# Optimization experiments

Hardware: AMD Instinct MI355X
Metric: run time of the kernel (lower is better)

Reference implementation:

```python
import jax, jax.numpy as jnp
import numpy as np

NUM_TOTAL = 150000
NUM_USER = 50000
NUM_ITEM = NUM_TOTAL - NUM_USER
D = 128
SOC_L = 2
CO_L = 2
NEG = 10
R = 0.7
E_SOC = 1600000
E_CO = 3200000
B = 512
MAX_UI = 64
MAX_IU = 50
W = 32
HOP = 3


def _sage_lgcn(x, src, dst, w, n, layers):
    # SAGEConv with edge-softmax weights over destination (LGCN 'mean' option).
    m = jax.lax.stop_gradient(jax.ops.segment_max(w, dst, num_segments=n))
    e = jnp.exp(w - m[dst])
    s = jax.ops.segment_sum(e, dst, num_segments=n)
    alpha = e / (s[dst] + 1e-16)
    for _ in range(layers):
        x = jax.ops.segment_sum(alpha[:, None] * x[src], dst, num_segments=n)
    return x  # LGCN.forward returns the last conv output (not the averaged sum)


def _sym_lgcn(x, src, dst, n, layers):
    # LGCConv: gcn_norm with added self-loops, symmetric D^-1/2 A D^-1/2.
    loop = jnp.arange(n)
    s2 = jnp.concatenate([src, loop])
    d2 = jnp.concatenate([dst, loop])
    deg = jax.ops.segment_sum(jnp.ones_like(d2, dtype=jnp.float32), d2, num_segments=n)
    dinv = jnp.where(deg > 0, deg ** -0.5, 0.0)
    ew = dinv[s2] * dinv[d2]
    for _ in range(layers):
        x = jax.ops.segment_sum(ew[:, None] * x[s2], d2, num_segments=n)
    return x


def _l2norm(x):
    return x / jnp.maximum(jnp.linalg.norm(x, axis=-1, keepdims=True), 1e-12)


def setup_inputs() -> dict:
    ks = jax.random.split(jax.random.key(0), 10)
    id_emb = 0.1 * jax.random.normal(ks[0], (NUM_TOTAL, D), jnp.float32)
    soc_id_emb = 0.1 * jax.random.normal(ks[1], (NUM_TOTAL, D), jnp.float32)
    soc_ext_weight = jax.random.uniform(ks[2], (E_SOC,), jnp.float32)
    soc_edge_index = jax.random.randint(ks[3], (2, E_SOC), 0, NUM_TOTAL)
    co_edge_index = jax.random.randint(ks[4], (2, E_CO), 0, NUM_TOTAL)
    uid = jax.random.randint(ks[5], (B,), 0, NUM_USER)
    pi = jax.random.randint(ks[9], (B,), NUM_USER, NUM_TOTAL)
    n_id = jnp.stack([uid, pi], axis=1)
    user_items = jax.random.randint(ks[6], (B, MAX_UI), 0, NUM_ITEM)
    item_users = jax.random.randint(ks[7], (NUM_ITEM, MAX_IU), 0, NUM_USER)
    walks = jax.random.randint(ks[8], (B, W, HOP), 0, NUM_TOTAL)
    return dict(id_emb=id_emb, soc_id_emb=soc_id_emb, soc_ext_weight=soc_ext_weight,
                soc_edge_index=soc_edge_index, co_edge_index=co_edge_index, n_id=n_id,
                user_items=user_items, item_users=item_users, walks=walks)


def reference(id_emb, soc_id_emb, soc_ext_weight, soc_edge_index, co_edge_index,
              n_id, user_items, item_users, walks):
    pi_id = n_id[:, 1]
    # two message-passing stacks
    soc_emb = _sage_lgcn(soc_id_emb, soc_edge_index[0], soc_edge_index[1],
                         soc_ext_weight, NUM_TOTAL, SOC_L)
    co_emb = _sym_lgcn(id_emb, co_edge_index[0], co_edge_index[1], NUM_TOTAL, CO_L)
    zero = jnp.zeros((1, D), id_emb.dtype)
    co_pad = jnp.concatenate([co_emb, zero], 0)
    soc_pad = jnp.concatenate([soc_emb, zero], 0)
    # vectorized per-user negative sampling: exclude interacted items, sample
    # NEG without replacement via top-k over masked uniform noise.
    rows = jnp.arange(B)[:, None]
    cols = jnp.where(user_items >= 0, user_items, 0)
    avail = jnp.ones((B, NUM_ITEM), jnp.int32).at[rows, cols].min(
        (user_items < 0).astype(jnp.int32))
    noise = jax.random.uniform(jax.random.key(42), (B, NUM_ITEM))
    scorez = jnp.where(avail > 0, noise, -1.0)
    _, neg_local = jax.lax.top_k(scorez, NEG)
    cand = jnp.concatenate([pi_id[:, None], neg_local + NUM_USER], axis=1)  # [B, 1+NEG]
    # item anchor soc embedding = mean of soc_emb over interacting users
    iu_idx = jnp.where(item_users >= 0, item_users, NUM_TOTAL)  # pad -> zero row
    cnt = (item_users >= 0).sum(-1, keepdims=True).astype(id_emb.dtype) + 1e-7
    anchor = soc_pad[iu_idx].sum(1) / cnt  # [NUM_ITEM, D]
    u_ref = jnp.concatenate([soc_emb[:NUM_USER], anchor, zero], 0)  # [NUM_TOTAL+1, D]
    co_n = _l2norm(co_pad)
    soc_n = _l2norm(u_ref)
    wk = walks.reshape(B, -1)  # [B, W*HOP]
    co_sim = (jnp.einsum('bcd,bwd->bcw', co_n[cand], co_n[wk]) + 1.0) * 0.5
    soc_sim = (jnp.einsum('bcd,bwd->bcw', soc_n[cand], soc_n[wk]) + 1.0) * 0.5
    return R * co_sim.mean(-1) + (1.0 - R) * soc_sim.mean(-1)  # [B, 1+NEG]
```

## Files before the change

kernel.cpp:

```cpp
#include <hip/hip_runtime.h>
#include <hip/hip_fp16.h>
#include <stdint.h>

#define NUM_TOTAL 150000
#define NUM_USER  50000
#define NUM_ITEM  100000
#define E_SOC 1600000
#define E_CO  3200000
#define BATCH 512
#define MAX_UI 64
#define MAX_IU 50
#define NWALK 96
#define NCAND 11
#define NB    586
#define NWG   192
#define PARTS 4
#define PIT   25000
#define PMW   784
#define SCAP  192
#define TH    8377900u

__device__ __forceinline__ uint32_t rotl32(uint32_t x, int r){ return (x<<r)|(x>>(32-r)); }

__device__ __forceinline__ void tf_core(uint32_t x0, uint32_t x1, uint32_t& o0, uint32_t& o1){
  const uint32_t k0 = 0u, k1 = 42u, k2 = 0u ^ 42u ^ 0x1BD11BDAu;
  x0 += k0; x1 += k1;
#define TF_R4(a,b,c,d) \
  x0+=x1; x1=rotl32(x1,a); x1^=x0; \
  x0+=x1; x1=rotl32(x1,b); x1^=x0; \
  x0+=x1; x1=rotl32(x1,c); x1^=x0; \
  x0+=x1; x1=rotl32(x1,d); x1^=x0;
  TF_R4(13,15,26,6)   x0+=k1; x1+=k2+1u;
  TF_R4(17,29,16,24)  x0+=k2; x1+=k0+2u;
  TF_R4(13,15,26,6)   x0+=k0; x1+=k1+3u;
  TF_R4(17,29,16,24)  x0+=k1; x1+=k2+4u;
  TF_R4(13,15,26,6)   x0+=k2; x1+=k0+5u;
#undef TF_R4
  o0 = x0; o1 = x1;
}

__device__ __forceinline__ uint32_t tf_bits(uint32_t j){
  uint32_t o0, o1;
  tf_core(0u, j, o0, o1);
  return o0 ^ o1;
}

__global__ __launch_bounds__(256) void pcountB_k(const int* __restrict__ socDst,
                                                 const int* __restrict__ coDst,
                                                 int chunkS, int chunkC,
                                                 int* __restrict__ cntMatS,
                                                 int* __restrict__ cntMatC){
  __shared__ int h[NB];
  int tid = threadIdx.x;
  bool isSoc = blockIdx.x < NWG;
  int wg = isSoc ? blockIdx.x : blockIdx.x - NWG;
  const int* dst = isSoc ? socDst : coDst;
  int E = isSoc ? E_SOC : E_CO;
  int chunk = isSoc ? chunkS : chunkC;
  int* cntMat = isSoc ? cntMatS : cntMatC;
  for (int i=tid; i<NB; i+=256) h[i]=0;
  __syncthreads();
  int lo = wg*chunk, hi = lo+chunk; if (hi > E) hi = E;
  for (int i=lo+tid; i<hi; i+=256) atomicAdd(&h[dst[i]>>8], 1);
  __syncthreads();
  for (int i=tid; i<NB; i+=256) cntMat[(size_t)i*NWG + wg] = h[i];
}

__global__ void btot2_k(const int* __restrict__ cntMatS, const int* __restrict__ cntMatC,
                        int* __restrict__ totS, int* __restrict__ totC){
  int g = (blockIdx.x*blockDim.x + threadIdx.x) >> 6;
  int lane = threadIdx.x & 63;
  if (g >= 2*NB) return;
  bool isSoc = g < NB;
  int b = isSoc ? g : g - NB;
  const int* row = (isSoc ? cntMatS : cntMatC) + (size_t)b*NWG;
  int s = row[lane*3] + row[lane*3+1] + row[lane*3+2];
  #pragma unroll
  for (int d=32; d; d>>=1) s += __shfl_xor(s, d, 64);
  if (lane == 0) (isSoc ? totS : totC)[b] = s;
}

__global__ __launch_bounds__(1024) void bscan2_k(const int* __restrict__ totS, const int* __restrict__ totC,
                                                 int* __restrict__ bbaseS, int* __restrict__ bbaseC){
  __shared__ int sa[1024];
  int tid = threadIdx.x;
  const int* tot = blockIdx.x ? totC : totS;
  int* bbase     = blockIdx.x ? bbaseC : bbaseS;
  int E          = blockIdx.x ? E_CO   : E_SOC;
  int v = (tid < NB) ? tot[tid] : 0;
  sa[tid] = v;
  __syncthreads();
  for (int s=1; s<1024; s<<=1){
    int t = (tid>=s)?sa[tid-s]:0;
    __syncthreads();
    sa[tid] += t;
    __syncthreads();
  }
  if (tid < NB) bbase[tid] = sa[tid] - v;
  if (tid == 0) bbase[NB] = E;
}

__global__ void wgpfx2_k(int* __restrict__ cntMatS, int* __restrict__ cntMatC,
                         const int* __restrict__ bbaseS, const int* __restrict__ bbaseC){
  int g = (blockIdx.x*blockDim.x + threadIdx.x) >> 6;
  int lane = threadIdx.x & 63;
  if (g >= 2*NB) return;
  bool isSoc = g < NB;
  int b = isSoc ? g : g - NB;
  int* row = (isSoc ? cntMatS : cntMatC) + (size_t)b*NWG;
  int base = (isSoc ? bbaseS : bbaseC)[b];
  int v0 = row[lane*3], v1 = row[lane*3+1], v2 = row[lane*3+2];
  int s = v0 + v1 + v2;
  int x = s;
  #pragma unroll
  for (int d=1; d<64; d<<=1){
    int t = __shfl_up(x, d, 64);
    if (lane >= d) x += t;
  }
  int excl = x - s;
  row[lane*3]   = base + excl;
  row[lane*3+1] = base + excl + v0;
  row[lane*3+2] = base + excl + v0 + v1;
}

__global__ __launch_bounds__(256) void pplaceB_k(const int* __restrict__ socSrc,
        const int* __restrict__ socDst, const float* __restrict__ socWgt,
        const int* __restrict__ coSrc,  const int* __restrict__ coDst,
        const int* __restrict__ cntMatS, const int* __restrict__ cntMatC,
        unsigned long long* __restrict__ recS, unsigned int* __restrict__ recC,
        int chunkS, int chunkC){
  __shared__ int curx[NB];
  int tid = threadIdx.x;
  bool isSoc = blockIdx.x < NWG;
  int wg = isSoc ? blockIdx.x : blockIdx.x - NWG;
  const int* offMat = isSoc ? cntMatS : cntMatC;
  for (int i=tid; i<NB; i+=256) curx[i] = offMat[(size_t)i*NWG + wg];
  __syncthreads();
  if (isSoc){
    int lo = wg*chunkS, hi = lo+chunkS; if (hi > E_SOC) hi = E_SOC;
    for (int i=lo+tid; i<hi; i+=256){
      int d = socDst[i];
      int p = atomicAdd(&curx[d>>8], 1);
      recS[p] = ((unsigned long long)__float_as_uint(socWgt[i])<<32)
              | (unsigned)(((d&255)<<18) | socSrc[i]);
    }
  } else {
    int lo = wg*chunkC, hi = lo+chunkC; if (hi > E_CO) hi = E_CO;
    for (int i=lo+tid; i<hi; i+=256){
      int d = coDst[i];
      int p = atomicAdd(&curx[d>>8], 1);
      recC[p] = (unsigned)(((d&255)<<18) | coSrc[i]);
    }
  }
}

__global__ __launch_bounds__(256) void cscB_k(const unsigned long long* __restrict__ recS,
    const unsigned int* __restrict__ recC,
    const int* __restrict__ bbaseS, const int* __restrict__ bbaseC,
    int* __restrict__ socOff, int* __restrict__ socSrcS, float* __restrict__ socWS,
    int* __restrict__ coOff, int* __restrict__ coSrcS, float* __restrict__ dinv){
  __shared__ int cnt[256], basex[256], curx[256];
  int tid = threadIdx.x;
  bool isSoc = blockIdx.x < NB;
  int b = isSoc ? blockIdx.x : blockIdx.x - NB;
  const int* bbase = isSoc ? bbaseS : bbaseC;
  int lo = bbase[b], hi = bbase[b+1];
  cnt[tid] = 0;
  __syncthreads();
  if (isSoc){
    for (int i = lo + tid; i < hi; i += 256)
      atomicAdd(&cnt[(((unsigned)recS[i]) >> 18) & 255], 1);
  } else {
    for (int i = lo + tid; i < hi; i += 256)
      atomicAdd(&cnt[(recC[i] >> 18) & 255], 1);
  }
  __syncthreads();
  int c = cnt[tid];
  basex[tid] = c; __syncthreads();
  for (int s=1; s<256; s<<=1){
    int t = (tid>=s)?basex[tid-s]:0; __syncthreads();
    basex[tid]+=t; __syncthreads();
  }
  int excl = basex[tid]-c;
  int node = b*256+tid;
  int* off = isSoc ? socOff : coOff;
  if (node <= NUM_TOTAL) off[node] = lo + excl;
  basex[tid] = excl; curx[tid] = 0;
  __syncthreads();
  if (isSoc){
    for (int i = lo + tid; i < hi; i += 256){
      unsigned long long r = recS[i];
      unsigned lw = (unsigned)r;
      int dl = (lw>>18)&255;
      int p = lo + basex[dl] + atomicAdd(&curx[dl],1);
      socSrcS[p] = lw & 0x3FFFF;
      socWS[p] = __uint_as_float((unsigned)(r>>32));
    }
    __syncthreads();
    if (node < NUM_TOTAL && c > 0){
      int e0 = lo + basex[tid], e1 = e0 + c;
      float m = -3.402823466e+38f;
      for (int e=e0; e<e1; ++e) m = fmaxf(m, socWS[e]);
      float s = 0.f;
      for (int e=e0; e<e1; ++e) s += expf(socWS[e] - m);
      float inv = 1.0f / (s + 1e-16f);
      for (int e=e0; e<e1; ++e) socWS[e] = expf(socWS[e] - m) * inv;
    }
  } else {
    for (int i = lo + tid; i < hi; i += 256){
      unsigned r = recC[i];
      int dl = (r>>18)&255;
      int p = lo + basex[dl] + atomicAdd(&curx[dl],1);
      coSrcS[p] = r & 0x3FFFF;
    }
    if (node < NUM_TOTAL) dinv[node] = 1.0f / sqrtf((float)(c + 1));
  }
}

__global__ __launch_bounds__(256) void negAf2h_k(const int* __restrict__ user_items,
        unsigned long long* __restrict__ surv, int* __restrict__ scnt,
        const float4* __restrict__ fa, uint2* __restrict__ oa,
        const float4* __restrict__ fb, uint2* __restrict__ ob, int n4){
  __shared__ unsigned int mask[PMW];
  __shared__ int lcnt;
  int tid = threadIdx.x;
  if (blockIdx.x < BATCH*PARTS){
    int blk = blockIdx.x;
    int row = blk >> 2, part = blk & 3;
    int base = part * PIT;
    for (int i=tid; i<PMW; i+=256) mask[i] = 0u;
    if (tid == 0) lcnt = 0;
    __syncthreads();
    if (tid < MAX_UI){
      int it = user_items[row*MAX_UI + tid];
      if (it >= base && it < base + PIT){
        int li = it - base;
        atomicOr(&mask[li>>5], 1u << (li & 31));
      }
    }
    __syncthreads();
    unsigned jbase = (unsigned)row * 100000u + (unsigned)base;
    for (int k = tid; k < PIT; k += 1024){
      int i1 = k + 256, i2 = k + 512, i3 = k + 768;
      uint32_t b0 = tf_bits(jbase + (unsigned)k);
      uint32_t b1 = tf_bits(jbase + (unsigned)(i1 < PIT ? i1 : k));
      uint32_t b2 = tf_bits(jbase + (unsigned)(i2 < PIT ? i2 : k));
      uint32_t b3 = tf_bits(jbase + (unsigned)(i3 < PIT ? i3 : k));
      uint32_t v0 = b0 >> 9, v1 = b1 >> 9, v2 = b2 >> 9, v3 = b3 >> 9;
      if (v0 >= TH && !((mask[k>>5] >> (k&31)) & 1u)){
        int p = atomicAdd(&lcnt, 1);
        if (p < SCAP)
          surv[(size_t)blk*SCAP + p] = ((unsigned long long)v0 << 32) | (unsigned)(~(unsigned)(base + k));
      }
      if (i1 < PIT && v1 >= TH && !((mask[i1>>5] >> (i1&31)) & 1u)){
        int p = atomicAdd(&lcnt, 1);
        if (p < SCAP)
          surv[(size_t)blk*SCAP + p] = ((unsigned long long)v1 << 32) | (unsigned)(~(unsigned)(base + i1));
      }
      if (i2 < PIT && v2 >= TH && !((mask[i2>>5] >> (i2&31)) & 1u)){
        int p = atomicAdd(&lcnt, 1);
        if (p < SCAP)
          surv[(size_t)blk*SCAP + p] = ((unsigned long long)v2 << 32) | (unsigned)(~(unsigned)(base + i2));
      }
      if (i3 < PIT && v3 >= TH && !((mask[i3>>5] >> (i3&31)) & 1u)){
        int p = atomicAdd(&lcnt, 1);
        if (p < SCAP)
          surv[(size_t)blk*SCAP + p] = ((unsigned long long)v3 << 32) | (unsigned)(~(unsigned)(base + i3));
      }
    }
    __syncthreads();
    if (tid == 0) scnt[blk] = (lcnt < SCAP) ? lcnt : SCAP;
  } else {
    int i = (int)(blockIdx.x - BATCH*PARTS)*256 + tid;
    int st = 2048*256;
    for (; i<n4; i+=st){
      float4 va = fa[i], vb = fb[i];
      __half2 l = __float22half2_rn(make_float2(va.x,va.y));
      __half2 h = __float22half2_rn(make_float2(va.z,va.w));
      uint2 u; u.x = *(unsigned*)&l; u.y = *(unsigned*)&h;
      oa[i] = u;
      l = __float22half2_rn(make_float2(vb.x,vb.y));
      h = __float22half2_rn(make_float2(vb.z,vb.w));
      u.x = *(unsigned*)&l; u.y = *(unsigned*)&h;
      ob[i] = u;
    }
  }
}

__global__ void agg_soc8_k(const __half2* __restrict__ x, __half2* __restrict__ y,
                           const int* __restrict__ off, const int* __restrict__ srcS,
                           const float* __restrict__ wE, int n){
  int gw = (blockIdx.x*blockDim.x + threadIdx.x) >> 6;
  int lane = threadIdx.x & 63;
  if (gw >= n) return;
  float ax = 0.f, ay = 0.f;
  int e = off[gw], e1 = off[gw+1];
  for (; e + 8 <= e1; e += 8){
    int s0=srcS[e],s1=srcS[e+1],s2=srcS[e+2],s3=srcS[e+3];
    int s4=srcS[e+4],s5=srcS[e+5],s6=srcS[e+6],s7=srcS[e+7];
    float a0=wE[e],a1=wE[e+1],a2=wE[e+2],a3=wE[e+3];
    float a4=wE[e+4],a5=wE[e+5],a6=wE[e+6],a7=wE[e+7];
    __half2 h0=x[(size_t)s0*64+lane], h1=x[(size_t)s1*64+lane];
    __half2 h2=x[(size_t)s2*64+lane], h3=x[(size_t)s3*64+lane];
    __half2 h4=x[(size_t)s4*64+lane], h5=x[(size_t)s5*64+lane];
    __half2 h6=x[(size_t)s6*64+lane], h7=x[(size_t)s7*64+lane];
    float2 f0=__half22float2(h0), f1=__half22float2(h1), f2=__half22float2(h2), f3=__half22float2(h3);
    float2 f4=__half22float2(h4), f5=__half22float2(h5), f6=__half22float2(h6), f7=__half22float2(h7);
    ax += a0*f0.x + a1*f1.x + a2*f2.x + a3*f3.x + a4*f4.x + a5*f5.x + a6*f6.x + a7*f7.x;
    ay += a0*f0.y + a1*f1.y + a2*f2.y + a3*f3.y + a4*f4.y + a5*f5.y + a6*f6.y + a7*f7.y;
  }
  for (; e < e1; ++e){
    int s = srcS[e]; float a = wE[e];
    float2 f = __half22float2(x[(size_t)s*64 + lane]);
    ax += a*f.x; ay += a*f.y;
  }
  y[(size_t)gw*64 + lane] = __float22half2_rn(make_float2(ax, ay));
}

__global__ void agg_co8_k(const __half2* __restrict__ x, __half2* __restrict__ y,
                          const int* __restrict__ off, const int* __restrict__ srcS,
                          const float* __restrict__ dinv, int n){
  int gw = (blockIdx.x*blockDim.x + threadIdx.x) >> 6;
  int lane = threadIdx.x & 63;
  if (gw >= n) return;
  float dv = dinv[gw];
  float2 fs = __half22float2(x[(size_t)gw*64 + lane]);
  float ax = dv*dv*fs.x, ay = dv*dv*fs.y;
  int e = off[gw], e1 = off[gw+1];
  for (; e + 8 <= e1; e += 8){
    int s0=srcS[e],s1=srcS[e+1],s2=srcS[e+2],s3=srcS[e+3];
    int s4=srcS[e+4],s5=srcS[e+5],s6=srcS[e+6],s7=srcS[e+7];
    float a0=dinv[s0]*dv,a1=dinv[s1]*dv,a2=dinv[s2]*dv,a3=dinv[s3]*dv;
    float a4=dinv[s4]*dv,a5=dinv[s5]*dv,a6=dinv[s6]*dv,a7=dinv[s7]*dv;
    __half2 h0=x[(size_t)s0*64+lane], h1=x[(size_t)s1*64+lane];
    __half2 h2=x[(size_t)s2*64+lane], h3=x[(size_t)s3*64+lane];
    __half2 h4=x[(size_t)s4*64+lane], h5=x[(size_t)s5*64+lane];
    __half2 h6=x[(size_t)s6*64+lane], h7=x[(size_t)s7*64+lane];
    float2 f0=__half22float2(h0), f1=__half22float2(h1), f2=__half22float2(h2), f3=__half22float2(h3);
    float2 f4=__half22float2(h4), f5=__half22float2(h5), f6=__half22float2(h6), f7=__half22float2(h7);
    ax += a0*f0.x + a1*f1.x + a2*f2.x + a3*f3.x + a4*f4.x + a5*f5.x + a6*f6.x + a7*f7.x;
    ay += a0*f0.y + a1*f1.y + a2*f2.y + a3*f3.y + a4*f4.y + a5*f5.y + a6*f6.y + a7*f7.y;
  }
  for (; e < e1; ++e){
    int s = srcS[e]; float a = dinv[s]*dv;
    float2 f = __half22float2(x[(size_t)s*64 + lane]);
    ax += a*f.x; ay += a*f.y;
  }
  y[(size_t)gw*64 + lane] = __float22half2_rn(make_float2(ax, ay));
}

__global__ void norm_h_k(__half2* __restrict__ x, int n){
  int gw = (blockIdx.x*blockDim.x + threadIdx.x) >> 6;
  int lane = threadIdx.x & 63;
  if (gw >= n) return;
  __half2* p = x + (size_t)gw*64;
  float2 v = __half22float2(p[lane]);
  float ss = v.x*v.x + v.y*v.y;
  #pragma unroll
  for (int s=32; s; s>>=1) ss += __shfl_xor(ss, s, 64);
  float sc = 1.0f / fmaxf(sqrtf(ss), 1e-12f);
  p[lane] = __float22half2_rn(make_float2(v.x*sc, v.y*sc));
}

__global__ void postA_k(__half2* __restrict__ coE, const __half2* __restrict__ socE,
                        const int* __restrict__ item_users, __half2* __restrict__ anch){
  int gw = (blockIdx.x*blockDim.x + threadIdx.x) >> 6;
  int lane = threadIdx.x & 63;
  if (gw < NUM_TOTAL){
    __half2* p = coE + (size_t)gw*64;
    float2 v = __half22float2(p[lane]);
    float ss = v.x*v.x + v.y*v.y;
    #pragma unroll
    for (int s=32; s; s>>=1) ss += __shfl_xor(ss, s, 64);
    float sc = 1.0f / fmaxf(sqrtf(ss), 1e-12f);
    p[lane] = __float22half2_rn(make_float2(v.x*sc, v.y*sc));
  } else {
    int it = gw - NUM_TOTAL;
    if (it >= NUM_ITEM) return;
    const int* us = item_users + (size_t)it*MAX_IU;
    float ax = 0.f, ay = 0.f;
    for (int k=0; k<MAX_IU; k+=10){
      int u0=us[k],u1=us[k+1],u2=us[k+2],u3=us[k+3],u4=us[k+4];
      int u5=us[k+5],u6=us[k+6],u7=us[k+7],u8=us[k+8],u9=us[k+9];
      __half2 h0=socE[(size_t)u0*64+lane], h1=socE[(size_t)u1*64+lane];
      __half2 h2=socE[(size_t)u2*64+lane], h3=socE[(size_t)u3*64+lane];
      __half2 h4=socE[(size_t)u4*64+lane], h5=socE[(size_t)u5*64+lane];
      __half2 h6=socE[(size_t)u6*64+lane], h7=socE[(size_t)u7*64+lane];
      __half2 h8=socE[(size_t)u8*64+lane], h9=socE[(size_t)u9*64+lane];
      float2 f0=__half22float2(h0), f1=__half22float2(h1), f2=__half22float2(h2);
      float2 f3=__half22float2(h3), f4=__half22float2(h4), f5=__half22float2(h5);
      float2 f6=__half22float2(h6), f7=__half22float2(h7), f8=__half22float2(h8);
      float2 f9=__half22float2(h9);
      ax += f0.x+f1.x+f2.x+f3.x+f4.x+f5.x+f6.x+f7.x+f8.x+f9.x;
      ay += f0.y+f1.y+f2.y+f3.y+f4.y+f5.y+f6.y+f7.y+f8.y+f9.y;
    }
    const float inv = 1.0f / (50.0f + 1e-7f);
    ax *= inv; ay *= inv;
    float ss = ax*ax + ay*ay;
    #pragma unroll
    for (int s=32; s; s>>=1) ss += __shfl_xor(ss, s, 64);
    float sc = 1.0f / fmaxf(sqrtf(ss), 1e-12f);
    anch[(size_t)it*64 + lane] = __float22half2_rn(make_float2(ax*sc, ay*sc));
  }
}

__global__ __launch_bounds__(256) void negB_k(const unsigned long long* __restrict__ surv,
                                              const int* __restrict__ scnt,
                                              const int* __restrict__ user_items,
                                              const int* __restrict__ n_id,
                                              int* __restrict__ cand){
  __shared__ unsigned long long keys[PARTS*SCAP];
  __shared__ unsigned long long red[256];
  __shared__ int cnts[PARTS];
  __shared__ int uix[MAX_UI];
  int b = blockIdx.x, tid = threadIdx.x;
  if (tid < PARTS) cnts[tid] = scnt[b*PARTS + tid];
  for (int i=tid; i<PARTS*SCAP; i+=256) keys[i] = 0ull;
  __syncthreads();
  int o0 = 0, o1 = cnts[0], o2 = o1 + cnts[1], o3 = o2 + cnts[2];
  int total = o3 + cnts[3];
  if (tid < cnts[0]) keys[o0 + tid] = surv[(size_t)(b*PARTS+0)*SCAP + tid];
  if (tid < cnts[1]) keys[o1 + tid] = surv[(size_t)(b*PARTS+1)*SCAP + tid];
  if (tid < cnts[2]) keys[o2 + tid] = surv[(size_t)(b*PARTS+2)*SCAP + tid];
  if (tid < cnts[3]) keys[o3 + tid] = surv[(size_t)(b*PARTS+3)*SCAP + tid];
  __syncthreads();
  if (total >= 10){
    for (int r=0; r<10; ++r){
      unsigned long long m = 0ull;
      for (int i=tid; i<PARTS*SCAP; i+=256){ unsigned long long v = keys[i]; if (v > m) m = v; }
      red[tid] = m; __syncthreads();
      for (int s=128; s>0; s>>=1){
        if (tid < s && red[tid+s] > red[tid]) red[tid] = red[tid+s];
        __syncthreads();
      }
      unsigned long long win = red[0];
      if (tid == 0)
        cand[b*NCAND + 1 + r] = NUM_USER + (int)(~(unsigned)(win & 0xffffffffull));
      for (int i=tid; i<PARTS*SCAP; i+=256) if (keys[i] == win) keys[i] = 0ull;
      __syncthreads();
    }
  } else {
    if (tid < MAX_UI) uix[tid] = user_items[b*MAX_UI + tid];
    __syncthreads();
    unsigned long long prev = ~0ull;
    for (int r=0; r<10; ++r){
      unsigned long long m = 0ull;
      for (int i=tid; i<NUM_ITEM; i+=256){
        bool msk = false;
        for (int j=0; j<MAX_UI; ++j) if (uix[j] == i) msk = true;
        if (msk) continue;
        uint32_t v = tf_bits((unsigned)b*100000u + (unsigned)i) >> 9;
        unsigned long long key = ((unsigned long long)v << 32) | (unsigned)(~(unsigned)i);
        if (key < prev && key > m) m = key;
      }
      red[tid] = m; __syncthreads();
      for (int s=128; s>0; s>>=1){
        if (tid < s && red[tid+s] > red[tid]) red[tid] = red[tid+s];
        __syncthreads();
      }
      unsigned long long win = red[0];
      prev = win;
      if (tid == 0)
        cand[b*NCAND + 1 + r] = NUM_USER + (int)(~(unsigned)(win & 0xffffffffull));
      __syncthreads();
    }
  }
  if (tid == 0) cand[b*NCAND] = n_id[b*2 + 1];
}

__global__ void sim_h_k(const __half2* __restrict__ coN, const __half2* __restrict__ socU,
                        const __half2* __restrict__ socI, const int* __restrict__ cand,
                        const int* __restrict__ walks, float* __restrict__ out){
  int b = blockIdx.x;
  int lane = threadIdx.x;
  float scx=0.f, scy=0.f, ssx=0.f, ssy=0.f;
  for (int w=0; w<NWALK; w+=4){
    int i0 = walks[b*NWALK + w],   i1 = walks[b*NWALK + w+1];
    int i2 = walks[b*NWALK + w+2], i3 = walks[b*NWALK + w+3];
    __half2 c0 = coN[(size_t)i0*64 + lane], c1 = coN[(size_t)i1*64 + lane];
    __half2 c2 = coN[(size_t)i2*64 + lane], c3 = coN[(size_t)i3*64 + lane];
    const __half2* p0 = (i0 < NUM_USER) ? socU + (size_t)i0*64 : socI + (size_t)(i0-NUM_USER)*64;
    const __half2* p1 = (i1 < NUM_USER) ? socU + (size_t)i1*64 : socI + (size_t)(i1-NUM_USER)*64;
    const __half2* p2 = (i2 < NUM_USER) ? socU + (size_t)i2*64 : socI + (size_t)(i2-NUM_USER)*64;
    const __half2* p3 = (i3 < NUM_USER) ? socU + (size_t)i3*64 : socI + (size_t)(i3-NUM_USER)*64;
    __half2 s0 = p0[lane], s1 = p1[lane], s2 = p2[lane], s3 = p3[lane];
    float2 fc0 = __half22float2(c0), fc1 = __half22float2(c1);
    float2 fc2 = __half22float2(c2), fc3 = __half22float2(c3);
    float2 fs0 = __half22float2(s0), fs1 = __half22float2(s1);
    float2 fs2 = __half22float2(s2), fs3 = __half22float2(s3);
    scx += fc0.x + fc1.x + fc2.x + fc3.x;
    scy += fc0.y + fc1.y + fc2.y + fc3.y;
    ssx += fs0.x + fs1.x + fs2.x + fs3.x;
    ssy += fs0.y + fs1.y + fs2.y + fs3.y;
  }
  for (int c=0; c<NCAND; ++c){
    int idx = cand[b*NCAND + c];
    float2 cv = __half22float2(coN[(size_t)idx*64 + lane]);
    float2 sv = __half22float2(socI[(size_t)(idx - NUM_USER)*64 + lane]);
    float dco = cv.x*scx + cv.y*scy;
    float dso = sv.x*ssx + sv.y*ssy;
    #pragma unroll
    for (int s=32; s; s>>=1){
      dco += __shfl_xor(dco, s, 64);
      dso += __shfl_xor(dso, s, 64);
    }
    if (lane == 0){
      float com = 0.5f + 0.5f*(dco / 96.0f);
      float som = 0.5f + 0.5f*(dso / 96.0f);
      out[b*NCAND + c] = 0.7f*com + 0.3f*som;
    }
  }
}

extern "C" void kernel_launch(void* const* d_in, const int* in_sizes, int n_in,
                              void* d_out, int out_size, void* d_ws, size_t ws_size,
                              hipStream_t stream){
  (void)in_sizes; (void)n_in; (void)out_size; (void)ws_size;
  const float* id_emb     = (const float*)d_in[0];
  const float* soc_id_emb = (const float*)d_in[1];
  const float* soc_w      = (const float*)d_in[2];
  const int*   soc_ei     = (const int*)d_in[3];
  const int*   co_ei      = (const int*)d_in[4];
  const int*   n_id       = (const int*)d_in[5];
  const int*   user_items = (const int*)d_in[6];
  const int*   item_users = (const int*)d_in[7];
  const int*   walks      = (const int*)d_in[8];
  float* out = (float*)d_out;

  char* w = (char*)d_ws;
  size_t cur = 0;
  auto take = [&](size_t bytes)->void*{
    void* p = w + cur;
    cur = (cur + bytes + 255) & ~(size_t)255;
    return p;
  };
  __half2* socId16 = (__half2*)take((size_t)NUM_TOTAL*64*4);
  __half2* id16    = (__half2*)take((size_t)NUM_TOTAL*64*4);
  __half2* t16     = (__half2*)take((size_t)NUM_TOTAL*64*4);
  __half2* soc16   = (__half2*)take((size_t)NUM_TOTAL*64*4);
  __half2* co16    = (__half2*)take((size_t)NUM_TOTAL*64*4);
  int*   socOff  = (int*)take((size_t)(NUM_TOTAL+1)*4);
  int*   coOff   = (int*)take((size_t)(NUM_TOTAL+1)*4);
  float* dinv    = (float*)take((size_t)NUM_TOTAL*4);
  int*   socSrcS = (int*)take((size_t)E_SOC*4);
  float* socWS   = (float*)take((size_t)E_SOC*4);
  int*   coSrcS  = (int*)take((size_t)E_CO*4);
  int*   cntMatS = (int*)take((size_t)NWG*NB*4);
  int*   cntMatC = (int*)take((size_t)NWG*NB*4);
  int*   bbaseS  = (int*)take((size_t)(NB+1)*4);
  int*   bbaseC  = (int*)take((size_t)(NB+1)*4);
  int*   totS    = (int*)take((size_t)NB*4);
  int*   totC    = (int*)take((size_t)NB*4);
  unsigned long long* surv = (unsigned long long*)take((size_t)BATCH*PARTS*SCAP*8);
  int*   scnt    = (int*)take((size_t)BATCH*PARTS*4);
  int*   cand    = (int*)take((size_t)BATCH*NCAND*4);

  unsigned long long* recS = (unsigned long long*)t16;
  unsigned int*       recC = (unsigned int*)((char*)t16 + (size_t)E_SOC*8);

  __half2* anch16 = socId16;

  const int T = 256;
  const int chunkS = (E_SOC + NWG - 1) / NWG;
  const int chunkC = (E_CO  + NWG - 1) / NWG;

  pcountB_k<<<2*NWG, T, 0, stream>>>(soc_ei + E_SOC, co_ei + E_CO, chunkS, chunkC, cntMatS, cntMatC);
  int scanGrid = (2*NB*64 + T - 1) / T;
  btot2_k<<<scanGrid, T, 0, stream>>>(cntMatS, cntMatC, totS, totC);
  bscan2_k<<<2, 1024, 0, stream>>>(totS, totC, bbaseS, bbaseC);
  wgpfx2_k<<<scanGrid, T, 0, stream>>>(cntMatS, cntMatC, bbaseS, bbaseC);
  pplaceB_k<<<2*NWG, T, 0, stream>>>(soc_ei, soc_ei + E_SOC, soc_w,
                                     co_ei, co_ei + E_CO,
                                     cntMatS, cntMatC, recS, recC, chunkS, chunkC);
  cscB_k<<<2*NB, T, 0, stream>>>(recS, recC, bbaseS, bbaseC,
                                 socOff, socSrcS, socWS, coOff, coSrcS, dinv);

  negAf2h_k<<<BATCH*PARTS + 2048, T, 0, stream>>>(user_items, surv, scnt,
                                 (const float4*)soc_id_emb, (uint2*)socId16,
                                 (const float4*)id_emb,     (uint2*)id16, NUM_TOTAL*32);

  int aggGrid = (NUM_TOTAL + 3) / 4;
  agg_soc8_k<<<aggGrid, T, 0, stream>>>(socId16, soc16, socOff, socSrcS, socWS, NUM_TOTAL);
  agg_soc8_k<<<aggGrid, T, 0, stream>>>(soc16,   t16,   socOff, socSrcS, socWS, NUM_TOTAL);
  agg_co8_k <<<aggGrid, T, 0, stream>>>(id16,    co16,  coOff,  coSrcS,  dinv,  NUM_TOTAL);
  agg_co8_k <<<aggGrid, T, 0, stream>>>(co16,    id16,  coOff,  coSrcS,  dinv,  NUM_TOTAL);

  __half2* socE = t16;
  __half2* coE  = id16;

  postA_k<<<(2*NUM_TOTAL - NUM_USER + 3)/4, T, 0, stream>>>(coE, socE, item_users, anch16);
  norm_h_k<<<(NUM_USER + 3)/4, T, 0, stream>>>(socE, NUM_USER);

  negB_k<<<BATCH, T, 0, stream>>>(surv, scnt, user_items, n_id, cand);
  sim_h_k<<<BATCH, 64, 0, stream>>>(coE, socE, anch16, cand, walks, out);
}
```

Measured before the change: 951.0 us.

## Fuse negative-sampling RNG blocks into co-graph aggregation kernels

The negative-sampling Threefry scoring blocks are split into two halves and interleaved, one in every 37 blocks, into the two co-graph aggregation launches. The f16 conversion becomes a standalone kernel, and the soc and co aggregation passes are reordered to alternate. The intent is to overlap the compute-heavy RNG work with the memory-bound gather aggregation instead of running it in a separate launch. The cost is more complex block index mapping, and the fused kernels may suffer from reduced occupancy or load imbalance.

```diff
diff --git a/kernel.cpp b/kernel.cpp
--- a/kernel.cpp
+++ b/kernel.cpp
@@ -19,6 +19,9 @@
 #define PMW   784
 #define SCAP  192
 #define TH    8377900u
+#define AGGGRID 37500
+#define NEGPER  1024
+#define ILP_P   37
 
 __device__ __forceinline__ uint32_t rotl32(uint32_t x, int r){ return (x<<r)|(x>>(32-r)); }
 
@@ -217,73 +220,19 @@
   }
 }
 
-__global__ __launch_bounds__(256) void negAf2h_k(const int* __restrict__ user_items,
-        unsigned long long* __restrict__ surv, int* __restrict__ scnt,
-        const float4* __restrict__ fa, uint2* __restrict__ oa,
-        const float4* __restrict__ fb, uint2* __restrict__ ob, int n4){
-  __shared__ unsigned int mask[PMW];
-  __shared__ int lcnt;
-  int tid = threadIdx.x;
-  if (blockIdx.x < BATCH*PARTS){
-    int blk = blockIdx.x;
-    int row = blk >> 2, part = blk & 3;
-    int base = part * PIT;
-    for (int i=tid; i<PMW; i+=256) mask[i] = 0u;
-    if (tid == 0) lcnt = 0;
-    __syncthreads();
-    if (tid < MAX_UI){
-      int it = user_items[row*MAX_UI + tid];
-      if (it >= base && it < base + PIT){
-        int li = it - base;
-        atomicOr(&mask[li>>5], 1u << (li & 31));
-      }
-    }
-    __syncthreads();
-    unsigned jbase = (unsigned)row * 100000u + (unsigned)base;
-    for (int k = tid; k < PIT; k += 1024){
-      int i1 = k + 256, i2 = k + 512, i3 = k + 768;
-      uint32_t b0 = tf_bits(jbase + (unsigned)k);
-      uint32_t b1 = tf_bits(jbase + (unsigned)(i1 < PIT ? i1 : k));
-      uint32_t b2 = tf_bits(jbase + (unsigned)(i2 < PIT ? i2 : k));
-      uint32_t b3 = tf_bits(jbase + (unsigned)(i3 < PIT ? i3 : k));
-      uint32_t v0 = b0 >> 9, v1 = b1 >> 9, v2 = b2 >> 9, v3 = b3 >> 9;
-      if (v0 >= TH && !((mask[k>>5] >> (k&31)) & 1u)){
-        int p = atomicAdd(&lcnt, 1);
-        if (p < SCAP)
-          surv[(size_t)blk*SCAP + p] = ((unsigned long long)v0 << 32) | (unsigned)(~(unsigned)(base + k));
-      }
-      if (i1 < PIT && v1 >= TH && !((mask[i1>>5] >> (i1&31)) & 1u)){
-        int p = atomicAdd(&lcnt, 1);
-        if (p < SCAP)
-          surv[(size_t)blk*SCAP + p] = ((unsigned long long)v1 << 32) | (unsigned)(~(unsigned)(base + i1));
-      }
-      if (i2 < PIT && v2 >= TH && !((mask[i2>>5] >> (i2&31)) & 1u)){
-        int p = atomicAdd(&lcnt, 1);
-        if (p < SCAP)
-          surv[(size_t)blk*SCAP + p] = ((unsigned long long)v2 << 32) | (unsigned)(~(unsigned)(base + i2));
-      }
-      if (i3 < PIT && v3 >= TH && !((mask[i3>>5] >> (i3&31)) & 1u)){
-        int p = atomicAdd(&lcnt, 1);
-        if (p < SCAP)
-          surv[(size_t)blk*SCAP + p] = ((unsigned long long)v3 << 32) | (unsigned)(~(unsigned)(base + i3));
-      }
-    }
-    __syncthreads();
-    if (tid == 0) scnt[blk] = (lcnt < SCAP) ? lcnt : SCAP;
-  } else {
-    int i = (int)(blockIdx.x - BATCH*PARTS)*256 + tid;
-    int st = 2048*256;
-    for (; i<n4; i+=st){
-      float4 va = fa[i], vb = fb[i];
-      __half2 l = __float22half2_rn(make_float2(va.x,va.y));
-      __half2 h = __float22half2_rn(make_float2(va.z,va.w));
-      uint2 u; u.x = *(unsigned*)&l; u.y = *(unsigned*)&h;
-      oa[i] = u;
-      l = __float22half2_rn(make_float2(vb.x,vb.y));
-      h = __float22half2_rn(make_float2(vb.z,vb.w));
-      u.x = *(unsigned*)&l; u.y = *(unsigned*)&h;
-      ob[i] = u;
-    }
+__global__ void f2h2_k(const float4* __restrict__ a, uint2* __restrict__ oa,
+                       const float4* __restrict__ b, uint2* __restrict__ ob, int n4){
+  int i = blockIdx.x*blockDim.x+threadIdx.x, st = gridDim.x*blockDim.x;
+  for (; i<n4; i+=st){
+    float4 va = a[i], vb = b[i];
+    __half2 l = __float22half2_rn(make_float2(va.x,va.y));
+    __half2 h = __float22half2_rn(make_float2(va.z,va.w));
+    uint2 u; u.x = *(unsigned*)&l; u.y = *(unsigned*)&h;
+    oa[i] = u;
+    l = __float22half2_rn(make_float2(vb.x,vb.y));
+    h = __float22half2_rn(make_float2(vb.z,vb.w));
+    u.x = *(unsigned*)&l; u.y = *(unsigned*)&h;
+    ob[i] = u;
   }
 }
 
@@ -317,36 +266,94 @@
   y[(size_t)gw*64 + lane] = __float22half2_rn(make_float2(ax, ay));
 }
 
-__global__ void agg_co8_k(const __half2* __restrict__ x, __half2* __restrict__ y,
+__global__ __launch_bounds__(256) void aggco_negA_k(const __half2* __restrict__ x, __half2* __restrict__ y,
                           const int* __restrict__ off, const int* __restrict__ srcS,
-                          const float* __restrict__ dinv, int n){
-  int gw = (blockIdx.x*blockDim.x + threadIdx.x) >> 6;
-  int lane = threadIdx.x & 63;
-  if (gw >= n) return;
-  float dv = dinv[gw];
-  float2 fs = __half22float2(x[(size_t)gw*64 + lane]);
-  float ax = dv*dv*fs.x, ay = dv*dv*fs.y;
-  int e = off[gw], e1 = off[gw+1];
-  for (; e + 8 <= e1; e += 8){
-    int s0=srcS[e],s1=srcS[e+1],s2=srcS[e+2],s3=srcS[e+3];
-    int s4=srcS[e+4],s5=srcS[e+5],s6=srcS[e+6],s7=srcS[e+7];
-    float a0=dinv[s0]*dv,a1=dinv[s1]*dv,a2=dinv[s2]*dv,a3=dinv[s3]*dv;
-    float a4=dinv[s4]*dv,a5=dinv[s5]*dv,a6=dinv[s6]*dv,a7=dinv[s7]*dv;
-    __half2 h0=x[(size_t)s0*64+lane], h1=x[(size_t)s1*64+lane];
-    __half2 h2=x[(size_t)s2*64+lane], h3=x[(size_t)s3*64+lane];
-    __half2 h4=x[(size_t)s4*64+lane], h5=x[(size_t)s5*64+lane];
-    __half2 h6=x[(size_t)s6*64+lane], h7=x[(size_t)s7*64+lane];
-    float2 f0=__half22float2(h0), f1=__half22float2(h1), f2=__half22float2(h2), f3=__half22float2(h3);
-    float2 f4=__half22float2(h4), f5=__half22float2(h5), f6=__half22float2(h6), f7=__half22float2(h7);
-    ax += a0*f0.x + a1*f1.x + a2*f2.x + a3*f3.x + a4*f4.x + a5*f5.x + a6*f6.x + a7*f7.x;
-    ay += a0*f0.y + a1*f1.y + a2*f2.y + a3*f3.y + a4*f4.y + a5*f5.y + a6*f6.y + a7*f7.y;
-  }
-  for (; e < e1; ++e){
-    int s = srcS[e]; float a = dinv[s]*dv;
-    float2 f = __half22float2(x[(size_t)s*64 + lane]);
-    ax += a*f.x; ay += a*f.y;
-  }
-  y[(size_t)gw*64 + lane] = __float22half2_rn(make_float2(ax, ay));
+                          const float* __restrict__ dinv,
+                          const int* __restrict__ user_items,
+                          unsigned long long* __restrict__ surv, int* __restrict__ scnt,
+                          int negBase){
+  __shared__ unsigned int mask[PMW];
+  __shared__ int lcnt;
+  int bid = blockIdx.x, tid = threadIdx.x;
+  int q = bid / ILP_P;
+  bool isNeg = (bid % ILP_P == 17) && (q < NEGPER);
+  if (isNeg){
+    int blk = negBase + q;
+    int row = blk >> 2, part = blk & 3;
+    int base = part * PIT;
+    for (int i=tid; i<PMW; i+=256) mask[i] = 0u;
+    if (tid == 0) lcnt = 0;
+    __syncthreads();
+    if (tid < MAX_UI){
+      int it = user_items[row*MAX_UI + tid];
+      if (it >= base && it < base + PIT){
+        int li = it - base;
+        atomicOr(&mask[li>>5], 1u << (li & 31));
+      }
+    }
+    __syncthreads();
+    unsigned jbase = (unsigned)row * 100000u + (unsigned)base;
+    for (int k = tid; k < PIT; k += 1024){
+      int i1 = k + 256, i2 = k + 512, i3 = k + 768;
+      uint32_t b0 = tf_bits(jbase + (unsigned)k);
+      uint32_t b1 = tf_bits(jbase + (unsigned)(i1 < PIT ? i1 : k));
+      uint32_t b2 = tf_bits(jbase + (unsigned)(i2 < PIT ? i2 : k));
+      uint32_t b3 = tf_bits(jbase + (unsigned)(i3 < PIT ? i3 : k));
+      uint32_t v0 = b0 >> 9, v1 = b1 >> 9, v2 = b2 >> 9, v3 = b3 >> 9;
+      if (v0 >= TH && !((mask[k>>5] >> (k&31)) & 1u)){
+        int p = atomicAdd(&lcnt, 1);
+        if (p < SCAP)
+          surv[(size_t)blk*SCAP + p] = ((unsigned long long)v0 << 32) | (unsigned)(~(unsigned)(base + k));
+      }
+      if (i1 < PIT && v1 >= TH && !((mask[i1>>5] >> (i1&31)) & 1u)){
+        int p = atomicAdd(&lcnt, 1);
+        if (p < SCAP)
+          surv[(size_t)blk*SCAP + p] = ((unsigned long long)v1 << 32) | (unsigned)(~(unsigned)(base + i1));
+      }
+      if (i2 < PIT && v2 >= TH && !((mask[i2>>5] >> (i2&31)) & 1u)){
+        int p = atomicAdd(&lcnt, 1);
+        if (p < SCAP)
+          surv[(size_t)blk*SCAP + p] = ((unsigned long long)v2 << 32) | (unsigned)(~(unsigned)(base + i2));
+      }
+      if (i3 < PIT && v3 >= TH && !((mask[i3>>5] >> (i3&31)) & 1u)){
+        int p = atomicAdd(&lcnt, 1);
+        if (p < SCAP)
+          surv[(size_t)blk*SCAP + p] = ((unsigned long long)v3 << 32) | (unsigned)(~(unsigned)(base + i3));
+      }
+    }
+    __syncthreads();
+    if (tid == 0) scnt[blk] = (lcnt < SCAP) ? lcnt : SCAP;
+  } else {
+    int nneg = (bid > 17) ? min((bid - 18)/ILP_P + 1, NEGPER) : 0;
+    int aggId = bid - nneg;
+    int gw = aggId*4 + (tid >> 6);
+    int lane = tid & 63;
+    if (gw >= NUM_TOTAL) return;
+    float dv = dinv[gw];
+    float2 fs = __half22float2(x[(size_t)gw*64 + lane]);
+    float ax = dv*dv*fs.x, ay = dv*dv*fs.y;
+    int e = off[gw], e1 = off[gw+1];
+    for (; e + 8 <= e1; e += 8){
+      int s0=srcS[e],s1=srcS[e+1],s2=srcS[e+2],s3=srcS[e+3];
+      int s4=srcS[e+4],s5=srcS[e+5],s6=srcS[e+6],s7=srcS[e+7];
+      float a0=dinv[s0]*dv,a1=dinv[s1]*dv,a2=dinv[s2]*dv,a3=dinv[s3]*dv;
+      float a4=dinv[s4]*dv,a5=dinv[s5]*dv,a6=dinv[s6]*dv,a7=dinv[s7]*dv;
+      __half2 h0=x[(size_t)s0*64+lane], h1=x[(size_t)s1*64+lane];
+      __half2 h2=x[(size_t)s2*64+lane], h3=x[(size_t)s3*64+lane];
+      __half2 h4=x[(size_t)s4*64+lane], h5=x[(size_t)s5*64+lane];
+      __half2 h6=x[(size_t)s6*64+lane], h7=x[(size_t)s7*64+lane];
+      float2 f0=__half22float2(h0), f1=__half22float2(h1), f2=__half22float2(h2), f3=__half22float2(h3);
+      float2 f4=__half22float2(h4), f5=__half22float2(h5), f6=__half22float2(h6), f7=__half22float2(h7);
+      ax += a0*f0.x + a1*f1.x + a2*f2.x + a3*f3.x + a4*f4.x + a5*f5.x + a6*f6.x + a7*f7.x;
+      ay += a0*f0.y + a1*f1.y + a2*f2.y + a3*f3.y + a4*f4.y + a5*f5.y + a6*f6.y + a7*f7.y;
+    }
+    for (; e < e1; ++e){
+      int s = srcS[e]; float a = dinv[s]*dv;
+      float2 f = __half22float2(x[(size_t)s*64 + lane]);
+      ax += a*f.x; ay += a*f.y;
+    }
+    y[(size_t)gw*64 + lane] = __float22half2_rn(make_float2(ax, ay));
+  }
 }
 
 __global__ void norm_h_k(__half2* __restrict__ x, int n){
@@ -575,15 +582,16 @@
   cscB_k<<<2*NB, T, 0, stream>>>(recS, recC, bbaseS, bbaseC,
                                  socOff, socSrcS, socWS, coOff, coSrcS, dinv);
 
-  negAf2h_k<<<BATCH*PARTS + 2048, T, 0, stream>>>(user_items, surv, scnt,
-                                 (const float4*)soc_id_emb, (uint2*)socId16,
+  f2h2_k<<<2048, T, 0, stream>>>((const float4*)soc_id_emb, (uint2*)socId16,
                                  (const float4*)id_emb,     (uint2*)id16, NUM_TOTAL*32);
 
   int aggGrid = (NUM_TOTAL + 3) / 4;
   agg_soc8_k<<<aggGrid, T, 0, stream>>>(socId16, soc16, socOff, socSrcS, socWS, NUM_TOTAL);
-  agg_soc8_k<<<aggGrid, T, 0, stream>>>(soc16,   t16,   socOff, socSrcS, socWS, NUM_TOTAL);
-  agg_co8_k <<<aggGrid, T, 0, stream>>>(id16,    co16,  coOff,  coSrcS,  dinv,  NUM_TOTAL);
-  agg_co8_k <<<aggGrid, T, 0, stream>>>(co16,    id16,  coOff,  coSrcS,  dinv,  NUM_TOTAL);
+  aggco_negA_k<<<AGGGRID + NEGPER, T, 0, stream>>>(id16, co16, coOff, coSrcS, dinv,
+                                                   user_items, surv, scnt, 0);
+  agg_soc8_k<<<aggGrid, T, 0, stream>>>(soc16, t16, socOff, socSrcS, socWS, NUM_TOTAL);
+  aggco_negA_k<<<AGGGRID + NEGPER, T, 0, stream>>>(co16, id16, coOff, coSrcS, dinv,
+                                                   user_items, surv, scnt, NEGPER);
 
   __half2* socE = t16;
   __half2* coE  = id16;
```

Measured after the change: 961.7 us. Within noise of the previous version (+1.1%).
